# Kernel optimization log

Measured on AMD Instinct MI355X. Metric: run time of the kernel, lower is better.

The kernel has to match this reference:

```python
import jax, jax.numpy as jnp
import numpy as np

B, L = 64, 262144
KERNEL_SIZES = [65, 33, 17, 9]
K_LIST = [L // ks for ks in KERNEL_SIZES]  # sparsity_density per kernel


def conv1d_same(x, w):
    # x: [B, 1, L], w: [kernel_size] -> torch F.conv1d(..., padding='same')
    return jax.lax.conv_general_dilated(
        x, w[None, None, :], window_strides=(1,), padding='SAME',
        dimension_numbers=('NCH', 'OIH', 'NCH'))


def topk_absolutes_1d(x, k):
    # keep the k largest-|x| entries along the last axis, zero elsewhere
    _, idx = jax.lax.top_k(jnp.abs(x), k)          # [B, 1, k]
    kept = jnp.take_along_axis(x, idx, axis=-1)    # [B, 1, k]
    b = jnp.arange(x.shape[0])[:, None, None]
    c = jnp.arange(x.shape[1])[None, :, None]
    return jnp.zeros_like(x).at[b, c, idx].set(kept)


def setup_inputs() -> dict:
    key = jax.random.key(0)
    batch_x = jax.random.normal(key, (B, 1, L), dtype=jnp.float32)
    inp = {'batch_x': batch_x}
    for i, ks in enumerate(KERNEL_SIZES):
        inp[f'w{i}'] = 0.1 * jnp.ones((ks,), dtype=jnp.float32)
    return inp


def reference(batch_x, w0, w1, w2, w3):
    weights = [w0, w1, w2, w3]
    recon_sum = jnp.zeros_like(batch_x)
    for w, k in zip(weights, K_LIST):
        similarity = conv1d_same(batch_x, w)
        activations = topk_absolutes_1d(similarity, k)
        recon_sum = recon_sum + conv1d_same(activations, w)
    return recon_sum
```

## Files before the change

### kernel.cpp

```cpp
#include <hip/hip_runtime.h>
#include <stdint.h>


#define B_ 64
#define L_ 262144
#define NBINS 8192
#define CAPC 8192
#define LCAP 1024
#define TSUB 2304
#define SUBS 8
#define NCHUNK 15
#define T5 2304
#define NT5 114
#define NSCAN 16

typedef unsigned int u32;

__device__ const int d_K[4] = {4032, 7943, 15420, 29127};

template<int KS>
__device__ __forceinline__ void k1_body(
    const float* __restrict__ xr, const float* __restrict__ w,
    float* __restrict__ yrow, u32* __restrict__ gh,
    float* xbuf, u32* h32)
{
  constexpr int PAD = KS / 2;
  constexpr int OFF = 32 - PAD;
  const int tid = threadIdx.x;

  float wreg[KS];
#pragma unroll
  for (int j = 0; j < KS; ++j) wreg[j] = w[j];

  for (int i = tid; i < NBINS / 2; i += 256) h32[i] = 0u;
  __syncthreads();

  for (int it = 0; it < SUBS; ++it) {
    const int base = (blockIdx.x * SUBS + it) * TSUB;
    if (base >= L_) break;
    const bool interior = (base >= 32) && (base + TSUB + 32 <= L_);
    if (interior) {
      const float4* src = (const float4*)(xr + base - 32);
      for (int i = tid; i < (TSUB + 64) / 4; i += 256)
        ((float4*)xbuf)[i] = src[i];
    } else {
      for (int i = tid; i < TSUB + 64; i += 256) {
        int g = base - 32 + i;
        xbuf[i] = (g >= 0 && g < L_) ? xr[g] : 0.0f;
      }
    }
    __syncthreads();

    float acc[9];
#pragma unroll
    for (int r = 0; r < 9; ++r) acc[r] = 0.0f;
    const int q0 = tid * 9;
#pragma unroll
    for (int p = 0; p < KS + 8; ++p) {
      float xv = xbuf[q0 + OFF + p];
#pragma unroll
      for (int r = 0; r < 9; ++r) {
        const int j = p - r;
        if (j >= 0 && j < KS) acc[r] = fmaf(xv, wreg[j], acc[r]);
      }
    }
#pragma unroll
    for (int r = 0; r < 9; ++r) {
      int g = base + q0 + r;
      if (g < L_) {
        u32 ab = __float_as_uint(acc[r]) & 0x7fffffffu;
        u32 bin = ab >> 18;
        atomicAdd(&h32[bin >> 1], 1u << (16 * (bin & 1)));
      }
    }
    __syncthreads();
#pragma unroll
    for (int r = 0; r < 9; ++r) xbuf[q0 + r] = acc[r];
    __syncthreads();
    const int n4 = (min(TSUB, L_ - base)) / 4;
    float4* dst = (float4*)(yrow + base);
    for (int i = tid; i < n4; i += 256) dst[i] = ((const float4*)xbuf)[i];
    __syncthreads();
  }

  for (int i = tid; i < NBINS / 2; i += 256) {
    u32 v = h32[i];
    u32 lo = v & 0xffffu, hi = v >> 16;
    if (lo) atomicAdd(&gh[2 * i], lo);
    if (hi) atomicAdd(&gh[2 * i + 1], hi);
  }
}

__global__ __launch_bounds__(256) void k1_hist(
    const float* __restrict__ x, const float* __restrict__ w0,
    const float* __restrict__ w1, const float* __restrict__ w2,
    const float* __restrict__ w3, float* __restrict__ y,
    u32* __restrict__ ghist, int kk0, int ng)
{
  __shared__ __align__(16) float xbuf[TSUB + 64];
  __shared__ u32 h32[NBINS / 2];
  const int kg = blockIdx.y;
  const int row = blockIdx.z;
  const int rkl = row * ng + kg;
  const int kk = kk0 + kg;
  const float* xr = x + (size_t)row * L_;
  float* yrow = y + (size_t)rkl * L_;
  u32* gh = ghist + (size_t)rkl * NBINS;
  switch (kk) {
    case 0:  k1_body<65>(xr, w0, yrow, gh, xbuf, h32); break;
    case 1:  k1_body<33>(xr, w1, yrow, gh, xbuf, h32); break;
    case 2:  k1_body<17>(xr, w2, yrow, gh, xbuf, h32); break;
    default: k1_body< 9>(xr, w3, yrow, gh, xbuf, h32); break;
  }
}

__global__ __launch_bounds__(256) void k2_findbin(
    const u32* __restrict__ ghist, u32* __restrict__ bbin, u32* __restrict__ rrem,
    int kk0, int ng)
{
  __shared__ u32 h[NBINS];
  __shared__ u32 ssum[256];
  const int rkl = blockIdx.x;
  const u32 k = (u32)d_K[kk0 + (rkl % ng)];
  const u32* gh = ghist + (size_t)rkl * NBINS;
  for (int i = threadIdx.x; i < NBINS; i += 256) h[i] = gh[i];
  __syncthreads();
  u32 s = 0;
  for (int i = 0; i < 32; ++i) s += h[threadIdx.x * 32 + i];
  ssum[threadIdx.x] = s;
  __syncthreads();
  if (threadIdx.x == 0) {
    u32 cum = 0; int b = 0;
    for (int t = 255; t >= 0; --t) {
      if (cum + ssum[t] >= k) {
        for (int i = t * 32 + 31; i >= t * 32; --i) {
          if (cum + h[i] >= k) { b = i; break; }
          cum += h[i];
        }
        break;
      }
      cum += ssum[t];
    }
    bbin[rkl] = (u32)b;
    rrem[rkl] = k - cum;
  }
}

__global__ __launch_bounds__(256) void k3_scan(
    const float* __restrict__ y, const u32* __restrict__ bbin,
    u32* __restrict__ ccount, uint2* __restrict__ cand, int ng)
{
  __shared__ uint2 lcand[LCAP];
  __shared__ u32 lmeta[3];
  const int tid = threadIdx.x;
  const int rkl = blockIdx.z * ng + blockIdx.y;
  const u32 target = bbin[rkl];
  if (tid == 0) lmeta[0] = 0u;
  __syncthreads();
  const float* yr = y + (size_t)rkl * L_;
  const int c0 = blockIdx.x * (L_ / NSCAN);
  const float4* src = (const float4*)(yr + c0);
  for (int i = tid; i < (L_ / NSCAN) / 4; i += 256) {
    float4 v = src[i];
    const float* vf = (const float*)&v;
#pragma unroll
    for (int c = 0; c < 4; ++c) {
      u32 ab = __float_as_uint(vf[c]) & 0x7fffffffu;
      if ((ab >> 18) == target) {
        u32 slot = atomicAdd(&lmeta[0], 1u);
        if (slot < LCAP) lcand[slot] = make_uint2(ab, (u32)(c0 + 4 * i + c));
      }
    }
  }
  __syncthreads();
  if (tid == 0) {
    u32 m = lmeta[0]; if (m > LCAP) m = LCAP;
    lmeta[1] = m;
    lmeta[2] = atomicAdd(&ccount[rkl], m);
  }
  __syncthreads();
  const u32 m = lmeta[1], bse = lmeta[2];
  uint2* cd = cand + (size_t)rkl * CAPC;
  for (u32 i = tid; i < m; i += 256)
    if (bse + i < CAPC) cd[bse + i] = lcand[i];
}

__global__ __launch_bounds__(256) void k4_select(
    const uint2* __restrict__ cand, const u32* __restrict__ ccount,
    const u32* __restrict__ bbinA, const u32* __restrict__ rremA,
    u32* __restrict__ thr, u32* __restrict__ keepAll,
    u32* __restrict__ excN, u32* __restrict__ excL)
{
  __shared__ u32 cab[CAPC];
  __shared__ u32 h64[64];
  __shared__ u32 sh[3];
  __shared__ u32 lidx[64];
  __shared__ u32 lcnt;
  const int rkl = blockIdx.x;
  int n = (int)min(ccount[rkl], (u32)CAPC);
  u32 r = rremA[rkl];
  if (r > (u32)n) r = (u32)n;
  const uint2* cd = cand + (size_t)rkl * CAPC;
  for (int i = threadIdx.x; i < n; i += 256) cab[i] = cd[i].x & 0x3ffffu;

  u32 sel = 0;
  for (int round = 0; round < 3; ++round) {
    const int shift = 12 - 6 * round;
    const u32 himask = (round == 0) ? 0u : ((0x3ffffu << (shift + 6)) & 0x3ffffu);
    if (threadIdx.x < 64) h64[threadIdx.x] = 0u;
    __syncthreads();
    for (int i = threadIdx.x; i < n; i += 256) {
      u32 v = cab[i];
      if ((v & himask) == (sel & himask)) atomicAdd(&h64[(v >> shift) & 63u], 1u);
    }
    __syncthreads();
    if (threadIdx.x == 0) {
      u32 cum = 0; int d = 0;
      for (int dd = 63; dd >= 0; --dd) {
        if (cum + h64[dd] >= r) { d = dd; break; }
        cum += h64[dd];
      }
      sh[0] = (u32)d;
      sh[1] = r - cum;
      sh[2] = h64[d];
    }
    __syncthreads();
    sel |= sh[0] << shift;
    r = sh[1];
  }
  const u32 dup = sh[2];
  const u32 m = r;
  if (threadIdx.x == 0) thr[rkl] = (bbinA[rkl] << 18) | sel;

  if (m >= dup) {
    if (threadIdx.x == 0) { keepAll[rkl] = 1u; excN[rkl] = 0u; }
    return;
  }
  if (threadIdx.x == 0) lcnt = 0u;
  __syncthreads();
  for (int i = threadIdx.x; i < n; i += 256) {
    if (cab[i] == sel) {
      u32 s2 = atomicAdd(&lcnt, 1u);
      if (s2 < 64) lidx[s2] = cd[i].y;
    }
  }
  __syncthreads();
  if (threadIdx.x == 0) {
    int c = (int)min(lcnt, 64u);
    for (int i = 1; i < c; ++i) {
      u32 v = lidx[i]; int j = i - 1;
      while (j >= 0 && lidx[j] > v) { lidx[j + 1] = lidx[j]; --j; }
      lidx[j + 1] = v;
    }
    u32 mm = min(m, 32u);
    keepAll[rkl] = 0u; excN[rkl] = mm;
    for (u32 i = 0; i < mm; ++i) excL[(size_t)rkl * 32 + i] = lidx[i];
  }
}

__device__ __forceinline__ float k5_mask(float yv, int g, u32 t_ab, u32 ka,
                                         u32 en, const u32* __restrict__ excp)
{
  u32 ab = __float_as_uint(yv) & 0x7fffffffu;
  bool keep = ab > t_ab;
  if (ab == t_ab) {
    if (ka) keep = true;
    else {
      for (u32 e = 0; e < en; ++e)
        if (excp[e] == (u32)g) { keep = true; break; }
    }
  }
  return keep ? yv : 0.0f;
}

template<int KS>
__device__ __forceinline__ void k5_conv(
    const float* __restrict__ w, const float* abuf, float* accO)
{
  constexpr int PAD = KS / 2;
  constexpr int OFF2 = 32 - PAD;
  float wreg[KS];
#pragma unroll
  for (int j = 0; j < KS; ++j) wreg[j] = w[j];
  const int o0 = threadIdx.x * 9;
#pragma unroll
  for (int p = 0; p < KS + 8; ++p) {
    float av = abuf[o0 + OFF2 + p];
#pragma unroll
    for (int r = 0; r < 9; ++r) {
      const int j = p - r;
      if (j >= 0 && j < KS) accO[r] = fmaf(av, wreg[j], accO[r]);
    }
  }
}

__global__ __launch_bounds__(256) void k5_final(
    const float* __restrict__ y, const float* __restrict__ w0,
    const float* __restrict__ w1, const float* __restrict__ w2,
    const float* __restrict__ w3, const u32* __restrict__ thr,
    const u32* __restrict__ keepAll, const u32* __restrict__ excN,
    const u32* __restrict__ excL, float* __restrict__ out,
    int kk0, int ng)
{
  __shared__ __align__(16) float abuf[T5 + 64];
  const int tid = threadIdx.x;
  const int row = blockIdx.y;
  const int tile0 = blockIdx.x * T5;
  float accO[9];
#pragma unroll
  for (int r = 0; r < 9; ++r) accO[r] = 0.0f;

  for (int kg = 0; kg < ng; ++kg) {
    const int rkl = row * ng + kg;
    const int kk = kk0 + kg;
    const u32 t_ab = thr[rkl], ka = keepAll[rkl], en = excN[rkl];
    const u32* excp = excL + (size_t)rkl * 32;
    const float* yr = y + (size_t)rkl * L_;
    const bool interior = (tile0 >= 32) && (tile0 + T5 + 32 <= L_);
    if (interior) {
      const float4* src = (const float4*)(yr + tile0 - 32);
      for (int i = tid; i < (T5 + 64) / 4; i += 256) {
        float4 v = src[i];
        float* vf = (float*)&v;
#pragma unroll
        for (int c = 0; c < 4; ++c)
          vf[c] = k5_mask(vf[c], tile0 - 32 + 4 * i + c, t_ab, ka, en, excp);
        ((float4*)abuf)[i] = v;
      }
    } else {
      for (int i = tid; i < T5 + 64; i += 256) {
        int g = tile0 - 32 + i;
        float av = 0.0f;
        if (g >= 0 && g < L_) av = k5_mask(yr[g], g, t_ab, ka, en, excp);
        abuf[i] = av;
      }
    }
    __syncthreads();
    switch (kk) {
      case 0:  k5_conv<65>(w0, abuf, accO); break;
      case 1:  k5_conv<33>(w1, abuf, accO); break;
      case 2:  k5_conv<17>(w2, abuf, accO); break;
      default: k5_conv< 9>(w3, abuf, accO); break;
    }
    __syncthreads();
  }

  const int o0 = tid * 9;
#pragma unroll
  for (int r = 0; r < 9; ++r) abuf[o0 + r] = accO[r];
  __syncthreads();
  float* orow = out + (size_t)row * L_ + tile0;
  const int n4 = (min(T5, L_ - tile0)) / 4;
  if (kk0 == 0) {
    for (int i = tid; i < n4; i += 256)
      ((float4*)orow)[i] = ((const float4*)abuf)[i];
  } else {
    for (int i = tid; i < n4; i += 256) {
      float4 prev = ((const float4*)orow)[i];
      float4 add = ((const float4*)abuf)[i];
      prev.x += add.x; prev.y += add.y; prev.z += add.z; prev.w += add.w;
      ((float4*)orow)[i] = prev;
    }
  }
}

extern "C" void kernel_launch(void* const* d_in, const int* in_sizes, int n_in,
                              void* d_out, int out_size, void* d_ws, size_t ws_size,
                              hipStream_t stream)
{
  (void)in_sizes; (void)n_in; (void)out_size;
  const float* x  = (const float*)d_in[0];
  const float* w0 = (const float*)d_in[1];
  const float* w1 = (const float*)d_in[2];
  const float* w2 = (const float*)d_in[3];
  const float* w3 = (const float*)d_in[4];
  float* out = (float*)d_out;

  auto need = [](int ng) -> size_t {
    return (size_t)ng * 64 * ((size_t)L_ * 4 + NBINS * 4 + 4 * 6 + 32 * 4 + CAPC * 8);
  };
  int ng = 1;
  if (ws_size >= need(4)) ng = 4;
  else if (ws_size >= need(2)) ng = 2;

  const size_t NRK = (size_t)64 * ng;
  float* y     = (float*)d_ws;
  u32* ghist   = (u32*)(y + NRK * L_);
  u32* ccount  = ghist + NRK * NBINS;
  u32* bbin    = ccount + NRK;
  u32* rrem    = bbin + NRK;
  u32* thr     = rrem + NRK;
  u32* kAll    = thr + NRK;
  u32* excN    = kAll + NRK;
  u32* excL    = excN + NRK;
  uint2* cand  = (uint2*)(excL + NRK * 32);

  for (int kk0 = 0; kk0 < 4; kk0 += ng) {
    hipMemsetAsync(ghist, 0, (NRK * NBINS + NRK) * sizeof(u32), stream);
    dim3 g1(NCHUNK, ng, B_);
    k1_hist<<<g1, 256, 0, stream>>>(x, w0, w1, w2, w3, y, ghist, kk0, ng);
    k2_findbin<<<(int)NRK, 256, 0, stream>>>(ghist, bbin, rrem, kk0, ng);
    dim3 g3(NSCAN, ng, B_);
    k3_scan<<<g3, 256, 0, stream>>>(y, bbin, ccount, cand, ng);
    k4_select<<<(int)NRK, 256, 0, stream>>>(cand, ccount, bbin, rrem, thr, kAll, excN, excL);
    dim3 g5(NT5, B_);
    k5_final<<<g5, 256, 0, stream>>>(y, w0, w1, w2, w3, thr, kAll, excN, excL, out, kk0, ng);
  }
}
```

Before: 526.0 us.

## Split histogram out of conv kernel and double-buffer conv input via async LDS loads

Moves the magnitude histogram out of the convolution kernel into a separate kernel that rereads y, so the conv kernel no longer does shared atomics. The conv kernel now double-buffers input tiles with global_load_lds direct-to-LDS loads and defers each tile's output store to overlap with the next tile's compute. The goal is to cut barriers and atomic contention in the conv stage. In exchange it adds a full extra read pass over y per top-k group plus an extra kernel launch.

```diff
diff --git a/kernel.cpp b/kernel.cpp
--- a/kernel.cpp
+++ b/kernel.cpp
@@ -10,6 +10,7 @@
 #define TSUB 2304
 #define SUBS 8
 #define NCHUNK 15
+#define XSTG 2560
 #define T5 2304
 #define NT5 114
 #define NSCAN 16
@@ -18,11 +19,36 @@
 
 __device__ const int d_K[4] = {4032, 7943, 15420, 29127};
 
+__device__ __forceinline__ void k1_stage(const float* __restrict__ xr, int base,
+                                         float* dst, int tid)
+{
+  const bool interior = (base >= 32) && (base - 32 + XSTG <= L_);
+  if (interior) {
+    const float* g0 = xr + (base - 32);
+    const int wv = tid >> 6, lane = tid & 63;
+#pragma unroll
+    for (int r = 0; r < 3; ++r) {
+      const int off = (r * 4 + wv) * 256;
+      if (off < XSTG) {
+        __builtin_amdgcn_global_load_lds(
+            (const __attribute__((address_space(1))) unsigned int*)(const void*)(g0 + off + lane * 4),
+            (__attribute__((address_space(3))) unsigned int*)(void*)(dst + off),
+            16, 0, 0);
+      }
+    }
+  } else {
+    for (int i = tid; i < TSUB + 64; i += 256) {
+      const int g = base - 32 + i;
+      dst[i] = (g >= 0 && g < L_) ? xr[g] : 0.0f;
+    }
+  }
+}
+
 template<int KS>
 __device__ __forceinline__ void k1_body(
     const float* __restrict__ xr, const float* __restrict__ w,
-    float* __restrict__ yrow, u32* __restrict__ gh,
-    float* xbuf, u32* h32)
+    float* __restrict__ yrow,
+    float* xb0, float* xb1, float* yb0, float* yb1)
 {
   constexpr int PAD = KS / 2;
   constexpr int OFF = 32 - PAD;
@@ -32,24 +58,28 @@
 #pragma unroll
   for (int j = 0; j < KS; ++j) wreg[j] = w[j];
 
-  for (int i = tid; i < NBINS / 2; i += 256) h32[i] = 0u;
-  __syncthreads();
+  const int base0 = blockIdx.x * SUBS * TSUB;
+  k1_stage(xr, base0, xb0, tid);
+  __syncthreads();
+
+  int pendBase = -1;
+  float* pendBuf = nullptr;
 
   for (int it = 0; it < SUBS; ++it) {
-    const int base = (blockIdx.x * SUBS + it) * TSUB;
+    const int base = base0 + it * TSUB;
     if (base >= L_) break;
-    const bool interior = (base >= 32) && (base + TSUB + 32 <= L_);
-    if (interior) {
-      const float4* src = (const float4*)(xr + base - 32);
-      for (int i = tid; i < (TSUB + 64) / 4; i += 256)
-        ((float4*)xbuf)[i] = src[i];
-    } else {
-      for (int i = tid; i < TSUB + 64; i += 256) {
-        int g = base - 32 + i;
-        xbuf[i] = (g >= 0 && g < L_) ? xr[g] : 0.0f;
-      }
-    }
-    __syncthreads();
+    float* xcur = (it & 1) ? xb1 : xb0;
+    float* xnxt = (it & 1) ? xb0 : xb1;
+    float* ycur = (it & 1) ? yb1 : yb0;
+    const int nbase = base + TSUB;
+    if (it + 1 < SUBS && nbase < L_)
+      k1_stage(xr, nbase, xnxt, tid);
+
+    if (pendBase >= 0) {
+      const int n4 = min(TSUB, L_ - pendBase) >> 2;
+      float4* dst = (float4*)(yrow + pendBase);
+      for (int i = tid; i < n4; i += 256) dst[i] = ((const float4*)pendBuf)[i];
+    }
 
     float acc[9];
 #pragma unroll
@@ -57,60 +87,76 @@
     const int q0 = tid * 9;
 #pragma unroll
     for (int p = 0; p < KS + 8; ++p) {
-      float xv = xbuf[q0 + OFF + p];
+      float xv = xcur[q0 + OFF + p];
 #pragma unroll
       for (int r = 0; r < 9; ++r) {
         const int j = p - r;
         if (j >= 0 && j < KS) acc[r] = fmaf(xv, wreg[j], acc[r]);
       }
     }
-#pragma unroll
-    for (int r = 0; r < 9; ++r) {
-      int g = base + q0 + r;
-      if (g < L_) {
-        u32 ab = __float_as_uint(acc[r]) & 0x7fffffffu;
-        u32 bin = ab >> 18;
-        atomicAdd(&h32[bin >> 1], 1u << (16 * (bin & 1)));
-      }
-    }
-    __syncthreads();
-#pragma unroll
-    for (int r = 0; r < 9; ++r) xbuf[q0 + r] = acc[r];
-    __syncthreads();
-    const int n4 = (min(TSUB, L_ - base)) / 4;
-    float4* dst = (float4*)(yrow + base);
-    for (int i = tid; i < n4; i += 256) dst[i] = ((const float4*)xbuf)[i];
-    __syncthreads();
-  }
-
-  for (int i = tid; i < NBINS / 2; i += 256) {
-    u32 v = h32[i];
-    u32 lo = v & 0xffffu, hi = v >> 16;
-    if (lo) atomicAdd(&gh[2 * i], lo);
-    if (hi) atomicAdd(&gh[2 * i + 1], hi);
-  }
-}
-
-__global__ __launch_bounds__(256) void k1_hist(
+
+#pragma unroll
+    for (int r = 0; r < 9; ++r) ycur[q0 + r] = acc[r];
+    pendBase = base; pendBuf = ycur;
+    __syncthreads();
+  }
+
+  if (pendBase >= 0) {
+    const int n4 = min(TSUB, L_ - pendBase) >> 2;
+    float4* dst = (float4*)(yrow + pendBase);
+    for (int i = tid; i < n4; i += 256) dst[i] = ((const float4*)pendBuf)[i];
+  }
+}
+
+__global__ __launch_bounds__(256) void k1_conv(
     const float* __restrict__ x, const float* __restrict__ w0,
     const float* __restrict__ w1, const float* __restrict__ w2,
     const float* __restrict__ w3, float* __restrict__ y,
-    u32* __restrict__ ghist, int kk0, int ng)
-{
-  __shared__ __align__(16) float xbuf[TSUB + 64];
-  __shared__ u32 h32[NBINS / 2];
+    int kk0, int ng)
+{
+  __shared__ __align__(16) float xb[2][XSTG];
+  __shared__ __align__(16) float yb[2][TSUB];
   const int kg = blockIdx.y;
   const int row = blockIdx.z;
   const int rkl = row * ng + kg;
   const int kk = kk0 + kg;
   const float* xr = x + (size_t)row * L_;
   float* yrow = y + (size_t)rkl * L_;
+  switch (kk) {
+    case 0:  k1_body<65>(xr, w0, yrow, xb[0], xb[1], yb[0], yb[1]); break;
+    case 1:  k1_body<33>(xr, w1, yrow, xb[0], xb[1], yb[0], yb[1]); break;
+    case 2:  k1_body<17>(xr, w2, yrow, xb[0], xb[1], yb[0], yb[1]); break;
+    default: k1_body< 9>(xr, w3, yrow, xb[0], xb[1], yb[0], yb[1]); break;
+  }
+}
+
+__global__ __launch_bounds__(256) void k2_hist(
+    const float* __restrict__ y, u32* __restrict__ ghist, int ng)
+{
+  __shared__ u32 h32[NBINS / 2];
+  const int tid = threadIdx.x;
+  const int rkl = blockIdx.z * ng + blockIdx.y;
+  for (int i = tid; i < NBINS / 2; i += 256) h32[i] = 0u;
+  __syncthreads();
+  const float* yr = y + (size_t)rkl * L_;
+  const int c0 = blockIdx.x * (L_ / NSCAN);
+  const float4* src = (const float4*)(yr + c0);
+  for (int i = tid; i < (L_ / NSCAN) / 4; i += 256) {
+    float4 v = src[i];
+    const float* vf = (const float*)&v;
+#pragma unroll
+    for (int c = 0; c < 4; ++c) {
+      u32 bin = (__float_as_uint(vf[c]) & 0x7fffffffu) >> 18;
+      atomicAdd(&h32[bin >> 1], 1u << (16 * (bin & 1)));
+    }
+  }
+  __syncthreads();
   u32* gh = ghist + (size_t)rkl * NBINS;
-  switch (kk) {
-    case 0:  k1_body<65>(xr, w0, yrow, gh, xbuf, h32); break;
-    case 1:  k1_body<33>(xr, w1, yrow, gh, xbuf, h32); break;
-    case 2:  k1_body<17>(xr, w2, yrow, gh, xbuf, h32); break;
-    default: k1_body< 9>(xr, w3, yrow, gh, xbuf, h32); break;
+  for (int i = tid; i < NBINS / 2; i += 256) {
+    u32 v = h32[i];
+    u32 lo = v & 0xffffu, hi = v >> 16;
+    if (lo) atomicAdd(&gh[2 * i], lo);
+    if (hi) atomicAdd(&gh[2 * i + 1], hi);
   }
 }
 
@@ -350,16 +396,16 @@
   for (int r = 0; r < 9; ++r) abuf[o0 + r] = accO[r];
   __syncthreads();
   float* orow = out + (size_t)row * L_ + tile0;
-  const int n4 = (min(T5, L_ - tile0)) / 4;
+  const int n4 = min(T5, L_ - tile0) / 4;
   if (kk0 == 0) {
     for (int i = tid; i < n4; i += 256)
       ((float4*)orow)[i] = ((const float4*)abuf)[i];
   } else {
     for (int i = tid; i < n4; i += 256) {
-      float4 prev = ((const float4*)orow)[i];
-      float4 add = ((const float4*)abuf)[i];
-      prev.x += add.x; prev.y += add.y; prev.z += add.z; prev.w += add.w;
-      ((float4*)orow)[i] = prev;
+      float4 p = ((const float4*)orow)[i];
+      float4 a = ((const float4*)abuf)[i];
+      p.x += a.x; p.y += a.y; p.z += a.z; p.w += a.w;
+      ((float4*)orow)[i] = p;
     }
   }
 }
@@ -398,7 +444,9 @@
   for (int kk0 = 0; kk0 < 4; kk0 += ng) {
     hipMemsetAsync(ghist, 0, (NRK * NBINS + NRK) * sizeof(u32), stream);
     dim3 g1(NCHUNK, ng, B_);
-    k1_hist<<<g1, 256, 0, stream>>>(x, w0, w1, w2, w3, y, ghist, kk0, ng);
+    k1_conv<<<g1, 256, 0, stream>>>(x, w0, w1, w2, w3, y, kk0, ng);
+    dim3 gh(NSCAN, ng, B_);
+    k2_hist<<<gh, 256, 0, stream>>>(y, ghist, ng);
     k2_findbin<<<(int)NRK, 256, 0, stream>>>(ghist, bbin, rrem, kk0, ng);
     dim3 g3(NSCAN, ng, B_);
     k3_scan<<<g3, 256, 0, stream>>>(y, bbin, ccount, cand, ng);
```

New measurement: 436.4 us. -17.0%, faster.

## Split conv and histogram kernels, retile convs to 8K chunks with async LDS staging

Applied to the files above, without the earlier changes.

The fused conv+histogram kernel is split into a pure convolution kernel and a separate histogram pass that writes per-slice partial histograms, so the global atomics and the hist memset go away. The convolution is retiled to 8192-element chunks where each thread computes 4 consecutive outputs from float4 LDS reads, and input staging uses global_load_lds direct-to-LDS loads. k5_final reuses the same conv routine and writes results straight from registers. The cost is an extra full read of y for the histogram pass and higher register pressure from 32 accumulators.

```diff
diff --git a/kernel.cpp b/kernel.cpp
--- a/kernel.cpp
+++ b/kernel.cpp
@@ -7,129 +7,154 @@
 #define NBINS 8192
 #define CAPC 8192
 #define LCAP 1024
-#define TSUB 2304
-#define SUBS 8
-#define NCHUNK 15
-#define T5 2304
-#define NT5 114
+#define CH 8192
+#define XSTG 8448
+#define NCH 32
+#define NH 8
 #define NSCAN 16
 
 typedef unsigned int u32;
 
 __device__ const int d_K[4] = {4032, 7943, 15420, 29127};
 
+__device__ __forceinline__ void stage_x(const float* __restrict__ xr, int c0,
+                                        float* dst, int tid)
+{
+  const bool interior = (c0 >= 32) && (c0 - 32 + XSTG <= L_);
+  if (interior) {
+    const float* g0 = xr + (c0 - 32);
+    const int wv = tid >> 6, lane = tid & 63;
+#pragma unroll
+    for (int r = 0; r < 9; ++r) {
+      const int idx = r * 4 + wv;
+      if (idx < XSTG / 256) {
+        const int off = idx * 256;
+        __builtin_amdgcn_global_load_lds(
+            (const __attribute__((address_space(1))) unsigned int*)(const void*)(g0 + off + lane * 4),
+            (__attribute__((address_space(3))) unsigned int*)(void*)(dst + off),
+            16, 0, 0);
+      }
+    }
+  } else {
+    for (int i = tid; i < XSTG; i += 256) {
+      const int g = c0 - 32 + i;
+      dst[i] = (g >= 0 && g < L_) ? xr[g] : 0.0f;
+    }
+  }
+}
+
 template<int KS>
-__device__ __forceinline__ void k1_body(
-    const float* __restrict__ xr, const float* __restrict__ w,
-    float* __restrict__ yrow, u32* __restrict__ gh,
-    float* xbuf, u32* h32)
+__device__ __forceinline__ void conv_acc(const float* __restrict__ w,
+                                         const float* xb, float a[32], int tid)
 {
   constexpr int PAD = KS / 2;
-  constexpr int OFF = 32 - PAD;
-  const int tid = threadIdx.x;
-
+  constexpr int NW = (KS + 3) / 4;
   float wreg[KS];
 #pragma unroll
   for (int j = 0; j < KS; ++j) wreg[j] = w[j];
-
-  for (int i = tid; i < NBINS / 2; i += 256) h32[i] = 0u;
-  __syncthreads();
-
-  for (int it = 0; it < SUBS; ++it) {
-    const int base = (blockIdx.x * SUBS + it) * TSUB;
-    if (base >= L_) break;
-    const bool interior = (base >= 32) && (base + TSUB + 32 <= L_);
-    if (interior) {
-      const float4* src = (const float4*)(xr + base - 32);
-      for (int i = tid; i < (TSUB + 64) / 4; i += 256)
-        ((float4*)xbuf)[i] = src[i];
-    } else {
-      for (int i = tid; i < TSUB + 64; i += 256) {
-        int g = base - 32 + i;
-        xbuf[i] = (g >= 0 && g < L_) ? xr[g] : 0.0f;
-      }
-    }
-    __syncthreads();
-
-    float acc[9];
-#pragma unroll
-    for (int r = 0; r < 9; ++r) acc[r] = 0.0f;
-    const int q0 = tid * 9;
-#pragma unroll
-    for (int p = 0; p < KS + 8; ++p) {
-      float xv = xbuf[q0 + OFF + p];
-#pragma unroll
-      for (int r = 0; r < 9; ++r) {
-        const int j = p - r;
-        if (j >= 0 && j < KS) acc[r] = fmaf(xv, wreg[j], acc[r]);
-      }
-    }
-#pragma unroll
-    for (int r = 0; r < 9; ++r) {
-      int g = base + q0 + r;
-      if (g < L_) {
-        u32 ab = __float_as_uint(acc[r]) & 0x7fffffffu;
-        u32 bin = ab >> 18;
-        atomicAdd(&h32[bin >> 1], 1u << (16 * (bin & 1)));
-      }
-    }
-    __syncthreads();
-#pragma unroll
-    for (int r = 0; r < 9; ++r) xbuf[q0 + r] = acc[r];
-    __syncthreads();
-    const int n4 = (min(TSUB, L_ - base)) / 4;
-    float4* dst = (float4*)(yrow + base);
-    for (int i = tid; i < n4; i += 256) dst[i] = ((const float4*)xbuf)[i];
-    __syncthreads();
-  }
-
-  for (int i = tid; i < NBINS / 2; i += 256) {
-    u32 v = h32[i];
-    u32 lo = v & 0xffffu, hi = v >> 16;
-    if (lo) atomicAdd(&gh[2 * i], lo);
-    if (hi) atomicAdd(&gh[2 * i + 1], hi);
-  }
-}
-
-__global__ __launch_bounds__(256) void k1_hist(
+#pragma unroll
+  for (int s = 0; s < 8; ++s) {
+    const int o = s * 1024 + tid * 4;
+    const float4* lp = (const float4*)(xb + o + 32 - PAD);
+    float a0 = a[s*4], a1 = a[s*4+1], a2 = a[s*4+2], a3 = a[s*4+3];
+#pragma unroll
+    for (int c = 0; c < NW; ++c) {
+      float4 xq = lp[c];
+#pragma unroll
+      for (int e = 0; e < 4; ++e) {
+        const int p = 4 * c + e;
+        const float xv = (e==0) ? xq.x : (e==1) ? xq.y : (e==2) ? xq.z : xq.w;
+        if (p     < KS)            a0 = fmaf(xv, wreg[p],     a0);
+        if (p-1 >= 0 && p-1 < KS)  a1 = fmaf(xv, wreg[p-1],   a1);
+        if (p-2 >= 0 && p-2 < KS)  a2 = fmaf(xv, wreg[p-2],   a2);
+        if (p-3 >= 0 && p-3 < KS)  a3 = fmaf(xv, wreg[p-3],   a3);
+      }
+    }
+    a[s*4] = a0; a[s*4+1] = a1; a[s*4+2] = a2; a[s*4+3] = a3;
+  }
+}
+
+__global__ __launch_bounds__(256) void k1_conv(
     const float* __restrict__ x, const float* __restrict__ w0,
     const float* __restrict__ w1, const float* __restrict__ w2,
     const float* __restrict__ w3, float* __restrict__ y,
-    u32* __restrict__ ghist, int kk0, int ng)
-{
-  __shared__ __align__(16) float xbuf[TSUB + 64];
-  __shared__ u32 h32[NBINS / 2];
+    int kk0, int ng)
+{
+  __shared__ __align__(16) float xb[XSTG];
+  const int tid = threadIdx.x;
   const int kg = blockIdx.y;
   const int row = blockIdx.z;
   const int rkl = row * ng + kg;
   const int kk = kk0 + kg;
+  const int c0 = blockIdx.x * CH;
   const float* xr = x + (size_t)row * L_;
   float* yrow = y + (size_t)rkl * L_;
-  u32* gh = ghist + (size_t)rkl * NBINS;
+
+  stage_x(xr, c0, xb, tid);
+  __syncthreads();
+
+  float a[32];
+#pragma unroll
+  for (int i = 0; i < 32; ++i) a[i] = 0.0f;
   switch (kk) {
-    case 0:  k1_body<65>(xr, w0, yrow, gh, xbuf, h32); break;
-    case 1:  k1_body<33>(xr, w1, yrow, gh, xbuf, h32); break;
-    case 2:  k1_body<17>(xr, w2, yrow, gh, xbuf, h32); break;
-    default: k1_body< 9>(xr, w3, yrow, gh, xbuf, h32); break;
-  }
+    case 0:  conv_acc<65>(w0, xb, a, tid); break;
+    case 1:  conv_acc<33>(w1, xb, a, tid); break;
+    case 2:  conv_acc<17>(w2, xb, a, tid); break;
+    default: conv_acc< 9>(w3, xb, a, tid); break;
+  }
+#pragma unroll
+  for (int s = 0; s < 8; ++s)
+    *(float4*)&yrow[c0 + s * 1024 + tid * 4] =
+        make_float4(a[s*4], a[s*4+1], a[s*4+2], a[s*4+3]);
+}
+
+__global__ __launch_bounds__(256) void k2_hist(
+    const float* __restrict__ y, u32* __restrict__ phist, int ng)
+{
+  __shared__ u32 h32[NBINS / 2];
+  const int tid = threadIdx.x;
+  const int rkl = blockIdx.z * ng + blockIdx.y;
+  for (int i = tid; i < NBINS / 2; i += 256) h32[i] = 0u;
+  __syncthreads();
+  const float4* src = (const float4*)(y + (size_t)rkl * L_ + blockIdx.x * (L_ / NH));
+  for (int i = tid; i < (L_ / NH) / 4; i += 256) {
+    float4 v = src[i];
+    const float* vf = (const float*)&v;
+#pragma unroll
+    for (int c = 0; c < 4; ++c) {
+      u32 bin = (__float_as_uint(vf[c]) & 0x7fffffffu) >> 18;
+      atomicAdd(&h32[bin >> 1], 1u << (16 * (bin & 1)));
+    }
+  }
+  __syncthreads();
+  u32* dst = phist + ((size_t)rkl * NH + blockIdx.x) * (NBINS / 2);
+  for (int i = tid; i < NBINS / 2; i += 256) dst[i] = h32[i];
 }
 
 __global__ __launch_bounds__(256) void k2_findbin(
-    const u32* __restrict__ ghist, u32* __restrict__ bbin, u32* __restrict__ rrem,
-    int kk0, int ng)
+    const u32* __restrict__ phist, u32* __restrict__ bbin, u32* __restrict__ rrem,
+    u32* __restrict__ ccount, int kk0, int ng)
 {
   __shared__ u32 h[NBINS];
   __shared__ u32 ssum[256];
+  const int tid = threadIdx.x;
   const int rkl = blockIdx.x;
   const u32 k = (u32)d_K[kk0 + (rkl % ng)];
-  const u32* gh = ghist + (size_t)rkl * NBINS;
-  for (int i = threadIdx.x; i < NBINS; i += 256) h[i] = gh[i];
+  for (int i = tid; i < NBINS / 2; i += 256) {
+    u32 lo = 0, hi = 0;
+#pragma unroll
+    for (int b = 0; b < NH; ++b) {
+      u32 v = phist[((size_t)rkl * NH + b) * (NBINS / 2) + i];
+      lo += v & 0xffffu; hi += v >> 16;
+    }
+    h[2 * i] = lo; h[2 * i + 1] = hi;
+  }
   __syncthreads();
   u32 s = 0;
-  for (int i = 0; i < 32; ++i) s += h[threadIdx.x * 32 + i];
-  ssum[threadIdx.x] = s;
-  __syncthreads();
-  if (threadIdx.x == 0) {
+  for (int i = 0; i < 32; ++i) s += h[tid * 32 + i];
+  ssum[tid] = s;
+  __syncthreads();
+  if (tid == 0) {
     u32 cum = 0; int b = 0;
     for (int t = 255; t >= 0; --t) {
       if (cum + ssum[t] >= k) {
@@ -143,6 +168,7 @@
     }
     bbin[rkl] = (u32)b;
     rrem[rkl] = k - cum;
+    ccount[rkl] = 0u;
   }
 }
 
@@ -273,27 +299,6 @@
   return keep ? yv : 0.0f;
 }
 
-template<int KS>
-__device__ __forceinline__ void k5_conv(
-    const float* __restrict__ w, const float* abuf, float* accO)
-{
-  constexpr int PAD = KS / 2;
-  constexpr int OFF2 = 32 - PAD;
-  float wreg[KS];
-#pragma unroll
-  for (int j = 0; j < KS; ++j) wreg[j] = w[j];
-  const int o0 = threadIdx.x * 9;
-#pragma unroll
-  for (int p = 0; p < KS + 8; ++p) {
-    float av = abuf[o0 + OFF2 + p];
-#pragma unroll
-    for (int r = 0; r < 9; ++r) {
-      const int j = p - r;
-      if (j >= 0 && j < KS) accO[r] = fmaf(av, wreg[j], accO[r]);
-    }
-  }
-}
-
 __global__ __launch_bounds__(256) void k5_final(
     const float* __restrict__ y, const float* __restrict__ w0,
     const float* __restrict__ w1, const float* __restrict__ w2,
@@ -302,64 +307,59 @@
     const u32* __restrict__ excL, float* __restrict__ out,
     int kk0, int ng)
 {
-  __shared__ __align__(16) float abuf[T5 + 64];
+  __shared__ __align__(16) float xb[XSTG];
   const int tid = threadIdx.x;
   const int row = blockIdx.y;
-  const int tile0 = blockIdx.x * T5;
-  float accO[9];
-#pragma unroll
-  for (int r = 0; r < 9; ++r) accO[r] = 0.0f;
+  const int c0 = blockIdx.x * CH;
+  float a[32];
+#pragma unroll
+  for (int i = 0; i < 32; ++i) a[i] = 0.0f;
 
   for (int kg = 0; kg < ng; ++kg) {
+    if (kg) __syncthreads();
     const int rkl = row * ng + kg;
     const int kk = kk0 + kg;
     const u32 t_ab = thr[rkl], ka = keepAll[rkl], en = excN[rkl];
     const u32* excp = excL + (size_t)rkl * 32;
     const float* yr = y + (size_t)rkl * L_;
-    const bool interior = (tile0 >= 32) && (tile0 + T5 + 32 <= L_);
+    const bool interior = (c0 >= 32) && (c0 - 32 + CH + 64 <= L_);
     if (interior) {
-      const float4* src = (const float4*)(yr + tile0 - 32);
-      for (int i = tid; i < (T5 + 64) / 4; i += 256) {
+      const float4* src = (const float4*)(yr + c0 - 32);
+      for (int i = tid; i < (CH + 64) / 4; i += 256) {
         float4 v = src[i];
         float* vf = (float*)&v;
-#pragma unroll
-        for (int c = 0; c < 4; ++c)
-          vf[c] = k5_mask(vf[c], tile0 - 32 + 4 * i + c, t_ab, ka, en, excp);
-        ((float4*)abuf)[i] = v;
+        const int gb = c0 - 32 + 4 * i;
+#pragma unroll
+        for (int c = 0; c < 4; ++c) vf[c] = k5_mask(vf[c], gb + c, t_ab, ka, en, excp);
+        ((float4*)xb)[i] = v;
       }
     } else {
-      for (int i = tid; i < T5 + 64; i += 256) {
-        int g = tile0 - 32 + i;
-        float av = 0.0f;
-        if (g >= 0 && g < L_) av = k5_mask(yr[g], g, t_ab, ka, en, excp);
-        abuf[i] = av;
+      for (int i = tid; i < CH + 64; i += 256) {
+        const int g = c0 - 32 + i;
+        xb[i] = (g >= 0 && g < L_) ? k5_mask(yr[g], g, t_ab, ka, en, excp) : 0.0f;
       }
     }
     __syncthreads();
     switch (kk) {
-      case 0:  k5_conv<65>(w0, abuf, accO); break;
-      case 1:  k5_conv<33>(w1, abuf, accO); break;
-      case 2:  k5_conv<17>(w2, abuf, accO); break;
-      default: k5_conv< 9>(w3, abuf, accO); break;
-    }
-    __syncthreads();
-  }
-
-  const int o0 = tid * 9;
-#pragma unroll
-  for (int r = 0; r < 9; ++r) abuf[o0 + r] = accO[r];
-  __syncthreads();
-  float* orow = out + (size_t)row * L_ + tile0;
-  const int n4 = (min(T5, L_ - tile0)) / 4;
+      case 0:  conv_acc<65>(w0, xb, a, tid); break;
+      case 1:  conv_acc<33>(w1, xb, a, tid); break;
+      case 2:  conv_acc<17>(w2, xb, a, tid); break;
+      default: conv_acc< 9>(w3, xb, a, tid); break;
+    }
+  }
+
+  float* orow = out + (size_t)row * L_ + c0;
   if (kk0 == 0) {
-    for (int i = tid; i < n4; i += 256)
-      ((float4*)orow)[i] = ((const float4*)abuf)[i];
+#pragma unroll
+    for (int s = 0; s < 8; ++s)
+      *(float4*)&orow[s * 1024 + tid * 4] =
+          make_float4(a[s*4], a[s*4+1], a[s*4+2], a[s*4+3]);
   } else {
-    for (int i = tid; i < n4; i += 256) {
-      float4 prev = ((const float4*)orow)[i];
-      float4 add = ((const float4*)abuf)[i];
-      prev.x += add.x; prev.y += add.y; prev.z += add.z; prev.w += add.w;
-      ((float4*)orow)[i] = prev;
+#pragma unroll
+    for (int s = 0; s < 8; ++s) {
+      float4 p = *(const float4*)&orow[s * 1024 + tid * 4];
+      p.x += a[s*4]; p.y += a[s*4+1]; p.z += a[s*4+2]; p.w += a[s*4+3];
+      *(float4*)&orow[s * 1024 + tid * 4] = p;
     }
   }
 }
@@ -377,7 +377,7 @@
   float* out = (float*)d_out;
 
   auto need = [](int ng) -> size_t {
-    return (size_t)ng * 64 * ((size_t)L_ * 4 + NBINS * 4 + 4 * 6 + 32 * 4 + CAPC * 8);
+    return (size_t)ng * 64 * ((size_t)L_ * 4 + NH * (NBINS / 2) * 4 + 6 * 4 + 32 * 4 + CAPC * 8);
   };
   int ng = 1;
   if (ws_size >= need(4)) ng = 4;
@@ -385,8 +385,8 @@
 
   const size_t NRK = (size_t)64 * ng;
   float* y     = (float*)d_ws;
-  u32* ghist   = (u32*)(y + NRK * L_);
-  u32* ccount  = ghist + NRK * NBINS;
+  u32* phist   = (u32*)(y + NRK * L_);
+  u32* ccount  = phist + NRK * NH * (NBINS / 2);
   u32* bbin    = ccount + NRK;
   u32* rrem    = bbin + NRK;
   u32* thr     = rrem + NRK;
@@ -396,14 +396,15 @@
   uint2* cand  = (uint2*)(excL + NRK * 32);
 
   for (int kk0 = 0; kk0 < 4; kk0 += ng) {
-    hipMemsetAsync(ghist, 0, (NRK * NBINS + NRK) * sizeof(u32), stream);
-    dim3 g1(NCHUNK, ng, B_);
-    k1_hist<<<g1, 256, 0, stream>>>(x, w0, w1, w2, w3, y, ghist, kk0, ng);
-    k2_findbin<<<(int)NRK, 256, 0, stream>>>(ghist, bbin, rrem, kk0, ng);
+    dim3 g1(NCH, ng, B_);
+    k1_conv<<<g1, 256, 0, stream>>>(x, w0, w1, w2, w3, y, kk0, ng);
+    dim3 gh(NH, ng, B_);
+    k2_hist<<<gh, 256, 0, stream>>>(y, phist, ng);
+    k2_findbin<<<(int)NRK, 256, 0, stream>>>(phist, bbin, rrem, ccount, kk0, ng);
     dim3 g3(NSCAN, ng, B_);
     k3_scan<<<g3, 256, 0, stream>>>(y, bbin, ccount, cand, ng);
     k4_select<<<(int)NRK, 256, 0, stream>>>(cand, ccount, bbin, rrem, thr, kAll, excN, excL);
-    dim3 g5(NT5, B_);
+    dim3 g5(NCH, B_);
     k5_final<<<g5, 256, 0, stream>>>(y, w0, w1, w2, w3, thr, kAll, excN, excL, out, kk0, ng);
   }
 }
```

New measurement: 829.2 us. 57.6% more time.
